# Kernel tuning notes

Measured on AMD Instinct MI355X. Metric: run time of the kernel, lower is better.

The kernel has to match this reference:

```python
import jax, jax.numpy as jnp
import numpy as np

B, S, IN_C, OUT_C = 2, 1024, 4096, 32000


def setup_inputs() -> dict:
    key = jax.random.key(0)
    k1, k2, k3 = jax.random.split(key, 3)
    hidden_states = jax.random.normal(k1, (B, S, IN_C), dtype=jnp.float32)
    weight = jax.random.normal(k2, (OUT_C, IN_C), dtype=jnp.float32) * 0.02
    bias = jax.random.normal(k3, (OUT_C,), dtype=jnp.float32) * 0.02
    return {"hidden_states": hidden_states, "weight": weight, "bias": bias,
            "split_num": 2}


def reference(hidden_states, weight, bias, split_num):
    # SlicedLMHead: split in_features into `split_num` contiguous slices,
    # run each slice as a linear to outC, accumulate, then add bias.
    in_c = hidden_states.shape[-1]
    split_size = in_c // split_num // 2 * 2
    logits = None
    for i in range(split_num):
        start = i * split_size
        end = (i + 1) * split_size if i < split_num - 1 else in_c
        h_slice = hidden_states[:, :, start:end]          # [B, S, slice]
        w_slice = weight[:, start:end]                    # [outC, slice]
        logits_slice = jnp.einsum('bsc,vc->bsv', h_slice, w_slice)
        logits = logits_slice if logits is None else logits + logits_slice
    return logits + bias
```

## Files before the change

kernel.cpp:

```cpp
#include <hip/hip_runtime.h>
#include <hip/hip_bf16.h>


typedef __attribute__((ext_vector_type(8))) short bhalf8;
typedef __attribute__((ext_vector_type(4))) float f32x4;
typedef __attribute__((ext_vector_type(8))) unsigned short us8;

#define M_DIM 2048
#define N_DIM 32000
#define K_DIM 4096
#define BM 256
#define BN 256
#define BK 64
#define NT (K_DIM / BK)
#define MBLKS (M_DIM / BM)
#define NBLKS (N_DIM / BN)
#define NWG (MBLKS * NBLKS)

#define W_ELEMS ((size_t)N_DIM * K_DIM)
#define H_ELEMS ((size_t)M_DIM * K_DIM)
#define WS_NEEDED ((W_ELEMS + H_ELEMS) * 2)

#define GLOAD_LDS16(g, l) \
    __builtin_amdgcn_global_load_lds( \
        (const __attribute__((address_space(1))) unsigned int*)(g), \
        (__attribute__((address_space(3))) unsigned int*)(l), 16, 0, 0)

__device__ __forceinline__ unsigned short f2bf_rn(float f) {
    unsigned int u = __float_as_uint(f);
    u += 0x7FFFu + ((u >> 16) & 1u);
    return (unsigned short)(u >> 16);
}

__global__ __launch_bounds__(256)
void cvt_f32_bf16(const float* __restrict__ in, unsigned short* __restrict__ out,
                  size_t n8) {
    size_t i = (size_t)blockIdx.x * blockDim.x + threadIdx.x;
    const size_t stride = (size_t)gridDim.x * blockDim.x;
    for (; i < n8; i += stride) {
        const float4 v0 = ((const float4*)in)[i * 2];
        const float4 v1 = ((const float4*)in)[i * 2 + 1];
        us8 p;
        p[0] = f2bf_rn(v0.x); p[1] = f2bf_rn(v0.y);
        p[2] = f2bf_rn(v0.z); p[3] = f2bf_rn(v0.w);
        p[4] = f2bf_rn(v1.x); p[5] = f2bf_rn(v1.y);
        p[6] = f2bf_rn(v1.z); p[7] = f2bf_rn(v1.w);
        ((us8*)out)[i] = p;
    }
}

__global__ __launch_bounds__(512, 2)
void lmhead_gemm_256(const unsigned short* __restrict__ A,
                     const unsigned short* __restrict__ W,
                     const float* __restrict__ bias,
                     float* __restrict__ C)
{
    __shared__ unsigned short lds[65536];

    const int tid  = threadIdx.x;
    const int bid  = blockIdx.x;
    const int wgid = (bid & 7) * (NWG / 8) + (bid >> 3);
    const int mblk = wgid & (MBLKS - 1);
    const int nblk = wgid >> 3;

    const int lane = tid & 63;
    const int wv   = tid >> 6;
    const int wr   = wv >> 2;
    const int wc   = wv & 3;
    const int l15  = lane & 15;
    const int l4   = lane >> 4;

    const int strow = tid >> 3;
    const int sgsw  = ((tid & 7) ^ (strow & 7)) << 3;
    const unsigned short* const srcA = A + (size_t)(mblk * BM + strow) * K_DIM + sgsw;
    const unsigned short* const srcB = W + (size_t)(nblk * BN + strow) * K_DIM + sgsw;
    const int dstw = (tid & 448) * 8;

#define STAGE_A(u, h) { \
        const unsigned short* s_ = srcA + (size_t)((h) * 128) * K_DIM + (size_t)(u) * BK; \
        unsigned short* d_ = &lds[((((u) & 1) * 2 + (h)) * 8192) + dstw]; \
        GLOAD_LDS16(s_, d_); GLOAD_LDS16(s_ + (size_t)64 * K_DIM, d_ + 4096); }
#define STAGE_B(u, h) { \
        const unsigned short* s_ = srcB + (size_t)((h) * 128) * K_DIM + (size_t)(u) * BK; \
        unsigned short* d_ = &lds[32768 + ((((u) & 1) * 2 + (h)) * 8192) + dstw]; \
        GLOAD_LDS16(s_, d_); GLOAD_LDS16(s_ + (size_t)64 * K_DIM, d_ + 4096); }

    const int swz0  = (l4 ^ (l15 & 7)) << 3;
    const int swz1  = ((4 + l4) ^ (l15 & 7)) << 3;
    const int aoff0 = l15 * 64 + swz0;
    const int aoff1 = l15 * 64 + swz1;
    const int boff0 = ((wc & 1) * 64 + l15) * 64 + swz0;
    const int boff1 = ((wc & 1) * 64 + l15) * 64 + swz1;

    f32x4 acc[8][4] = {};
    bhalf8 af0[4][2], af1[4][2], bf[4][2];

    STAGE_A(0, 0); STAGE_A(0, 1);
    STAGE_B(0, 0); STAGE_B(0, 1);
    STAGE_A(1, 0); STAGE_A(1, 1);
    asm volatile("s_waitcnt vmcnt(4)" ::: "memory");
    __builtin_amdgcn_sched_barrier(0);
    __builtin_amdgcn_s_barrier();

    for (int t = 0; t < NT; ++t) {
        const int b = t & 1;
        const unsigned short* asb = &lds[(b * 2 + wr) * 8192];
        const unsigned short* bsb = &lds[32768 + (b * 2 + (wc >> 1)) * 8192];

        #pragma unroll
        for (int mf = 0; mf < 4; ++mf) {
            af0[mf][0] = *(const bhalf8*)&asb[aoff0 + mf * 1024];
            af0[mf][1] = *(const bhalf8*)&asb[aoff1 + mf * 1024];
        }
        #pragma unroll
        for (int nf = 0; nf < 2; ++nf) {
            bf[nf][0] = *(const bhalf8*)&bsb[boff0 + nf * 1024];
            bf[nf][1] = *(const bhalf8*)&bsb[boff1 + nf * 1024];
        }
        if (t + 1 < NT) STAGE_B(t + 1, 0);
        __builtin_amdgcn_sched_barrier(0);
        __builtin_amdgcn_s_barrier();
        asm volatile("s_waitcnt lgkmcnt(0)" ::: "memory");
        __builtin_amdgcn_sched_barrier(0);
        __builtin_amdgcn_s_setprio(1);
        #pragma unroll
        for (int mf = 0; mf < 4; ++mf)
            #pragma unroll
            for (int nf = 0; nf < 2; ++nf)
                #pragma unroll
                for (int kk = 0; kk < 2; ++kk)
                    acc[mf][nf] = __builtin_amdgcn_mfma_f32_16x16x32_bf16(
                        af0[mf][kk], bf[nf][kk], acc[mf][nf], 0, 0, 0);
        __builtin_amdgcn_s_setprio(0);
        __builtin_amdgcn_s_barrier();

        #pragma unroll
        for (int nf = 0; nf < 2; ++nf) {
            bf[2 + nf][0] = *(const bhalf8*)&bsb[boff0 + (2 + nf) * 1024];
            bf[2 + nf][1] = *(const bhalf8*)&bsb[boff1 + (2 + nf) * 1024];
        }
        if (t + 1 < NT) STAGE_B(t + 1, 1);
        __builtin_amdgcn_sched_barrier(0);
        __builtin_amdgcn_s_barrier();
        asm volatile("s_waitcnt lgkmcnt(0)" ::: "memory");
        __builtin_amdgcn_sched_barrier(0);
        __builtin_amdgcn_s_setprio(1);
        #pragma unroll
        for (int mf = 0; mf < 4; ++mf)
            #pragma unroll
            for (int nf = 0; nf < 2; ++nf)
                #pragma unroll
                for (int kk = 0; kk < 2; ++kk)
                    acc[mf][2 + nf] = __builtin_amdgcn_mfma_f32_16x16x32_bf16(
                        af0[mf][kk], bf[2 + nf][kk], acc[mf][2 + nf], 0, 0, 0);
        __builtin_amdgcn_s_setprio(0);
        __builtin_amdgcn_s_barrier();

        #pragma unroll
        for (int mf = 0; mf < 4; ++mf) {
            af1[mf][0] = *(const bhalf8*)&asb[aoff0 + 4096 + mf * 1024];
            af1[mf][1] = *(const bhalf8*)&asb[aoff1 + 4096 + mf * 1024];
        }
        __builtin_amdgcn_sched_barrier(0);
        __builtin_amdgcn_s_barrier();
        asm volatile("s_waitcnt lgkmcnt(0)" ::: "memory");
        __builtin_amdgcn_sched_barrier(0);
        __builtin_amdgcn_s_setprio(1);
        #pragma unroll
        for (int mf = 0; mf < 4; ++mf)
            #pragma unroll
            for (int nf = 0; nf < 2; ++nf)
                #pragma unroll
                for (int kk = 0; kk < 2; ++kk)
                    acc[4 + mf][2 + nf] = __builtin_amdgcn_mfma_f32_16x16x32_bf16(
                        af1[mf][kk], bf[2 + nf][kk], acc[4 + mf][2 + nf], 0, 0, 0);
        __builtin_amdgcn_s_setprio(0);
        __builtin_amdgcn_s_barrier();

        if (t + 2 < NT) { STAGE_A(t + 2, 0); STAGE_A(t + 2, 1); }
        __builtin_amdgcn_sched_barrier(0);
        __builtin_amdgcn_s_barrier();
        __builtin_amdgcn_s_setprio(1);
        #pragma unroll
        for (int mf = 0; mf < 4; ++mf)
            #pragma unroll
            for (int nf = 0; nf < 2; ++nf)
                #pragma unroll
                for (int kk = 0; kk < 2; ++kk)
                    acc[4 + mf][nf] = __builtin_amdgcn_mfma_f32_16x16x32_bf16(
                        af1[mf][kk], bf[nf][kk], acc[4 + mf][nf], 0, 0, 0);
        __builtin_amdgcn_s_setprio(0);
        if (t < NT - 2) { asm volatile("s_waitcnt vmcnt(4)" ::: "memory"); }
        else            { asm volatile("s_waitcnt vmcnt(0)" ::: "memory"); }
        __builtin_amdgcn_sched_barrier(0);
        __builtin_amdgcn_s_barrier();
    }

    const size_t crow0 = (size_t)(mblk * BM + wr * 128 + l4 * 4);
    const int    ccol0 = nblk * BN + wc * 64 + l15;
    #pragma unroll
    for (int jn = 0; jn < 4; ++jn) {
        const float bv = bias[ccol0 + jn * 16];
        #pragma unroll
        for (int i = 0; i < 8; ++i) {
            const size_t base = (crow0 + (size_t)i * 16) * N_DIM + ccol0 + jn * 16;
            #pragma unroll
            for (int r = 0; r < 4; ++r)
                C[base + (size_t)r * N_DIM] = acc[i][jn][r] + bv;
        }
    }
#undef STAGE_A
#undef STAGE_B
}

__global__ __launch_bounds__(256, 2)
void lmhead_gemm_f32(const float* __restrict__ A, const float* __restrict__ W,
                     const float* __restrict__ bias, float* __restrict__ C) {
    __shared__ unsigned short As[2][128 * 64];
    __shared__ unsigned short Bs[2][128 * 64];

    const int tid  = threadIdx.x;
    const int bid  = blockIdx.x;
    const int mblk = bid & 15;
    const int nblk = bid >> 4;
    const int st_row = tid >> 3;
    const int st_g   = tid & 7;
    const int lane = tid & 63;
    const int wv   = tid >> 6;
    const int wm   = (wv >> 1) << 6;
    const int wn   = (wv & 1) << 6;
    const int l15  = lane & 15;
    const int l4   = lane >> 4;

    const float* aptr = A + (size_t)(mblk * 128 + st_row) * K_DIM + st_g * 8;
    const float* bptr = W + (size_t)(nblk * 128 + st_row) * K_DIM + st_g * 8;

    f32x4 acc[4][4] = {};
    float4 ra[4][2], rb[4][2];

    #pragma unroll
    for (int s = 0; s < 4; ++s) {
        const float* ap = aptr + (size_t)(s * 32) * K_DIM;
        const float* bp = bptr + (size_t)(s * 32) * K_DIM;
        ra[s][0] = *(const float4*)(ap);   ra[s][1] = *(const float4*)(ap + 4);
        rb[s][0] = *(const float4*)(bp);   rb[s][1] = *(const float4*)(bp + 4);
    }
    #pragma unroll
    for (int s = 0; s < 4; ++s) {
        const int row = s * 32 + st_row;
        const int off = row * 64 + ((st_g ^ (row & 7)) << 3);
        us8 pa, pb;
        #pragma unroll
        for (int j = 0; j < 4; ++j) {
            pa[j] = f2bf_rn(((const float*)&ra[s][0])[j]);
            pa[j + 4] = f2bf_rn(((const float*)&ra[s][1])[j]);
            pb[j] = f2bf_rn(((const float*)&rb[s][0])[j]);
            pb[j + 4] = f2bf_rn(((const float*)&rb[s][1])[j]);
        }
        *(us8*)&As[0][off] = pa;  *(us8*)&Bs[0][off] = pb;
    }
    __syncthreads();

    for (int t = 0; t < 64; ++t) {
        const int cur = t & 1;
        const bool more = (t + 1) < 64;
        if (more) {
            const float* ap = aptr + (size_t)(t + 1) * 64;
            const float* bp = bptr + (size_t)(t + 1) * 64;
            #pragma unroll
            for (int s = 0; s < 4; ++s) {
                ra[s][0] = *(const float4*)(ap + (size_t)(s * 32) * K_DIM);
                ra[s][1] = *(const float4*)(ap + (size_t)(s * 32) * K_DIM + 4);
                rb[s][0] = *(const float4*)(bp + (size_t)(s * 32) * K_DIM);
                rb[s][1] = *(const float4*)(bp + (size_t)(s * 32) * K_DIM + 4);
            }
        }
        const unsigned short* as = As[cur];
        const unsigned short* bs = Bs[cur];
        #pragma unroll
        for (int kk = 0; kk < 2; ++kk) {
            bhalf8 af[4], bfv[4];
            #pragma unroll
            for (int mf = 0; mf < 4; ++mf) {
                const int row = wm + mf * 16 + l15;
                af[mf] = *(const bhalf8*)&as[row * 64 + ((((kk << 2) + l4) ^ (row & 7)) << 3)];
            }
            #pragma unroll
            for (int nf = 0; nf < 4; ++nf) {
                const int row = wn + nf * 16 + l15;
                bfv[nf] = *(const bhalf8*)&bs[row * 64 + ((((kk << 2) + l4) ^ (row & 7)) << 3)];
            }
            #pragma unroll
            for (int mf = 0; mf < 4; ++mf)
                #pragma unroll
                for (int nf = 0; nf < 4; ++nf)
                    acc[mf][nf] = __builtin_amdgcn_mfma_f32_16x16x32_bf16(
                        af[mf], bfv[nf], acc[mf][nf], 0, 0, 0);
        }
        if (more) {
            const int nbuf = cur ^ 1;
            #pragma unroll
            for (int s = 0; s < 4; ++s) {
                const int row = s * 32 + st_row;
                const int off = row * 64 + ((st_g ^ (row & 7)) << 3);
                us8 pa, pb;
                #pragma unroll
                for (int j = 0; j < 4; ++j) {
                    pa[j] = f2bf_rn(((const float*)&ra[s][0])[j]);
                    pa[j + 4] = f2bf_rn(((const float*)&ra[s][1])[j]);
                    pb[j] = f2bf_rn(((const float*)&rb[s][0])[j]);
                    pb[j + 4] = f2bf_rn(((const float*)&rb[s][1])[j]);
                }
                *(us8*)&As[nbuf][off] = pa;  *(us8*)&Bs[nbuf][off] = pb;
            }
        }
        __syncthreads();
    }

    const size_t crow0 = (size_t)(mblk * 128 + wm + l4 * 4);
    const int    ccol0 = nblk * 128 + wn + l15;
    #pragma unroll
    for (int nf = 0; nf < 4; ++nf) {
        const float bv = bias[ccol0 + nf * 16];
        #pragma unroll
        for (int mf = 0; mf < 4; ++mf) {
            const size_t base = (crow0 + (size_t)mf * 16) * N_DIM + ccol0 + nf * 16;
            #pragma unroll
            for (int r = 0; r < 4; ++r)
                C[base + (size_t)r * N_DIM] = acc[mf][nf][r] + bv;
        }
    }
}

extern "C" void kernel_launch(void* const* d_in, const int* in_sizes, int n_in,
                              void* d_out, int out_size, void* d_ws, size_t ws_size,
                              hipStream_t stream) {
    const float* h = (const float*)d_in[0];
    const float* w = (const float*)d_in[1];
    const float* b = (const float*)d_in[2];
    float* out = (float*)d_out;

    if (ws_size >= WS_NEEDED) {
        unsigned short* wbf = (unsigned short*)d_ws;
        unsigned short* hbf = wbf + W_ELEMS;
        cvt_f32_bf16<<<2048, 256, 0, stream>>>(w, wbf, W_ELEMS / 8);
        cvt_f32_bf16<<<512, 256, 0, stream>>>(h, hbf, H_ELEMS / 8);
        lmhead_gemm_256<<<NWG, 512, 0, stream>>>(hbf, wbf, b, out);
    } else {
        lmhead_gemm_f32<<<4000, 256, 0, stream>>>(h, w, b, out);
    }
}
```

Measured before the change: 629.5 us.

## Restructure bf16 GEMM main loop into register double-buffered k-half pipeline

Replaces the four-phase per-tile schedule, which had many barriers and staggered A/B staging, with a two-half scheme. Fragments for the next k-half are read from LDS into a second register set while 32 MFMAs run on the current set. Whole tiles are staged two ahead, with one barrier per tile. The output is written with nontemporal stores to avoid polluting cache. This adds fragment registers, which risks spills or lower occupancy, and it waits vmcnt(0) every tile, which may expose global load latency.

Measured after the change: 1.998 ms. +217.4%, slower.

```diff
diff --git a/kernel.cpp b/kernel.cpp
--- a/kernel.cpp
+++ b/kernel.cpp
@@ -76,141 +76,101 @@
     const unsigned short* const srcB = W + (size_t)(nblk * BN + strow) * K_DIM + sgsw;
     const int dstw = (tid & 448) * 8;
 
-#define STAGE_A(u, h) { \
+#define STAGE_A(u, h, BUF) { \
         const unsigned short* s_ = srcA + (size_t)((h) * 128) * K_DIM + (size_t)(u) * BK; \
-        unsigned short* d_ = &lds[((((u) & 1) * 2 + (h)) * 8192) + dstw]; \
+        unsigned short* d_ = &lds[(((BUF) * 2 + (h)) * 8192) + dstw]; \
         GLOAD_LDS16(s_, d_); GLOAD_LDS16(s_ + (size_t)64 * K_DIM, d_ + 4096); }
-#define STAGE_B(u, h) { \
+#define STAGE_B(u, h, BUF) { \
         const unsigned short* s_ = srcB + (size_t)((h) * 128) * K_DIM + (size_t)(u) * BK; \
-        unsigned short* d_ = &lds[32768 + ((((u) & 1) * 2 + (h)) * 8192) + dstw]; \
+        unsigned short* d_ = &lds[32768 + (((BUF) * 2 + (h)) * 8192) + dstw]; \
         GLOAD_LDS16(s_, d_); GLOAD_LDS16(s_ + (size_t)64 * K_DIM, d_ + 4096); }
-
-    const int swz0  = (l4 ^ (l15 & 7)) << 3;
-    const int swz1  = ((4 + l4) ^ (l15 & 7)) << 3;
-    const int aoff0 = l15 * 64 + swz0;
-    const int aoff1 = l15 * 64 + swz1;
-    const int boff0 = ((wc & 1) * 64 + l15) * 64 + swz0;
-    const int boff1 = ((wc & 1) * 64 + l15) * 64 + swz1;
+#define STAGE_TILE(u, BUF) { \
+        STAGE_A(u, 0, BUF); STAGE_A(u, 1, BUF); \
+        STAGE_B(u, 0, BUF); STAGE_B(u, 1, BUF); }
+
+    const int swz0 = (l4 ^ (l15 & 7)) << 3;
+    const int swz1 = ((4 + l4) ^ (l15 & 7)) << 3;
+    const int arow = l15 * 64;
+    const int brow = ((wc & 1) * 64 + l15) * 64;
+
+    const unsigned short* const asp[2] = { &lds[wr * 8192],
+                                           &lds[(2 + wr) * 8192] };
+    const unsigned short* const bsp[2] = { &lds[32768 + (wc >> 1) * 8192],
+                                           &lds[32768 + (2 + (wc >> 1)) * 8192] };
 
     f32x4 acc[8][4] = {};
-    bhalf8 af0[4][2], af1[4][2], bf[4][2];
-
-    STAGE_A(0, 0); STAGE_A(0, 1);
-    STAGE_B(0, 0); STAGE_B(0, 1);
-    STAGE_A(1, 0); STAGE_A(1, 1);
-    asm volatile("s_waitcnt vmcnt(4)" ::: "memory");
+    bhalf8 aA[8], bA[4];
+    bhalf8 aB[8], bB[4];
+
+#define ISSUE_FRAGS(av, bv, as_, bs_, swz) { \
+        const unsigned short* _as = (as_); const unsigned short* _bs = (bs_); \
+        _Pragma("unroll") \
+        for (int i = 0; i < 4; ++i) av[i]     = *(const bhalf8*)&_as[arow + (swz) + i * 1024]; \
+        _Pragma("unroll") \
+        for (int i = 0; i < 4; ++i) av[4 + i] = *(const bhalf8*)&_as[arow + (swz) + 4096 + i * 1024]; \
+        _Pragma("unroll") \
+        for (int j = 0; j < 4; ++j) bv[j]     = *(const bhalf8*)&_bs[brow + (swz) + j * 1024]; }
+
+#define MFMA32(av, bv) { \
+        _Pragma("unroll") \
+        for (int i = 0; i < 8; ++i) \
+            _Pragma("unroll") \
+            for (int j = 0; j < 4; ++j) \
+                acc[i][j] = __builtin_amdgcn_mfma_f32_16x16x32_bf16(av[i], bv[j], acc[i][j], 0, 0, 0); }
+
+    STAGE_TILE(0, 0);
+    STAGE_TILE(1, 1);
+    asm volatile("s_waitcnt vmcnt(8)" ::: "memory");
     __builtin_amdgcn_sched_barrier(0);
     __builtin_amdgcn_s_barrier();
-
-    for (int t = 0; t < NT; ++t) {
-        const int b = t & 1;
-        const unsigned short* asb = &lds[(b * 2 + wr) * 8192];
-        const unsigned short* bsb = &lds[32768 + (b * 2 + (wc >> 1)) * 8192];
-
-        #pragma unroll
-        for (int mf = 0; mf < 4; ++mf) {
-            af0[mf][0] = *(const bhalf8*)&asb[aoff0 + mf * 1024];
-            af0[mf][1] = *(const bhalf8*)&asb[aoff1 + mf * 1024];
-        }
-        #pragma unroll
-        for (int nf = 0; nf < 2; ++nf) {
-            bf[nf][0] = *(const bhalf8*)&bsb[boff0 + nf * 1024];
-            bf[nf][1] = *(const bhalf8*)&bsb[boff1 + nf * 1024];
-        }
-        if (t + 1 < NT) STAGE_B(t + 1, 0);
-        __builtin_amdgcn_sched_barrier(0);
-        __builtin_amdgcn_s_barrier();
-        asm volatile("s_waitcnt lgkmcnt(0)" ::: "memory");
-        __builtin_amdgcn_sched_barrier(0);
-        __builtin_amdgcn_s_setprio(1);
-        #pragma unroll
-        for (int mf = 0; mf < 4; ++mf)
-            #pragma unroll
-            for (int nf = 0; nf < 2; ++nf)
-                #pragma unroll
-                for (int kk = 0; kk < 2; ++kk)
-                    acc[mf][nf] = __builtin_amdgcn_mfma_f32_16x16x32_bf16(
-                        af0[mf][kk], bf[nf][kk], acc[mf][nf], 0, 0, 0);
-        __builtin_amdgcn_s_setprio(0);
-        __builtin_amdgcn_s_barrier();
-
-        #pragma unroll
-        for (int nf = 0; nf < 2; ++nf) {
-            bf[2 + nf][0] = *(const bhalf8*)&bsb[boff0 + (2 + nf) * 1024];
-            bf[2 + nf][1] = *(const bhalf8*)&bsb[boff1 + (2 + nf) * 1024];
-        }
-        if (t + 1 < NT) STAGE_B(t + 1, 1);
-        __builtin_amdgcn_sched_barrier(0);
-        __builtin_amdgcn_s_barrier();
-        asm volatile("s_waitcnt lgkmcnt(0)" ::: "memory");
-        __builtin_amdgcn_sched_barrier(0);
-        __builtin_amdgcn_s_setprio(1);
-        #pragma unroll
-        for (int mf = 0; mf < 4; ++mf)
-            #pragma unroll
-            for (int nf = 0; nf < 2; ++nf)
-                #pragma unroll
-                for (int kk = 0; kk < 2; ++kk)
-                    acc[mf][2 + nf] = __builtin_amdgcn_mfma_f32_16x16x32_bf16(
-                        af0[mf][kk], bf[2 + nf][kk], acc[mf][2 + nf], 0, 0, 0);
-        __builtin_amdgcn_s_setprio(0);
-        __builtin_amdgcn_s_barrier();
-
-        #pragma unroll
-        for (int mf = 0; mf < 4; ++mf) {
-            af1[mf][0] = *(const bhalf8*)&asb[aoff0 + 4096 + mf * 1024];
-            af1[mf][1] = *(const bhalf8*)&asb[aoff1 + 4096 + mf * 1024];
-        }
-        __builtin_amdgcn_sched_barrier(0);
-        __builtin_amdgcn_s_barrier();
-        asm volatile("s_waitcnt lgkmcnt(0)" ::: "memory");
-        __builtin_amdgcn_sched_barrier(0);
-        __builtin_amdgcn_s_setprio(1);
-        #pragma unroll
-        for (int mf = 0; mf < 4; ++mf)
-            #pragma unroll
-            for (int nf = 0; nf < 2; ++nf)
-                #pragma unroll
-                for (int kk = 0; kk < 2; ++kk)
-                    acc[4 + mf][2 + nf] = __builtin_amdgcn_mfma_f32_16x16x32_bf16(
-                        af1[mf][kk], bf[2 + nf][kk], acc[4 + mf][2 + nf], 0, 0, 0);
-        __builtin_amdgcn_s_setprio(0);
-        __builtin_amdgcn_s_barrier();
-
-        if (t + 2 < NT) { STAGE_A(t + 2, 0); STAGE_A(t + 2, 1); }
-        __builtin_amdgcn_sched_barrier(0);
-        __builtin_amdgcn_s_barrier();
-        __builtin_amdgcn_s_setprio(1);
-        #pragma unroll
-        for (int mf = 0; mf < 4; ++mf)
-            #pragma unroll
-            for (int nf = 0; nf < 2; ++nf)
-                #pragma unroll
-                for (int kk = 0; kk < 2; ++kk)
-                    acc[4 + mf][nf] = __builtin_amdgcn_mfma_f32_16x16x32_bf16(
-                        af1[mf][kk], bf[nf][kk], acc[4 + mf][nf], 0, 0, 0);
-        __builtin_amdgcn_s_setprio(0);
-        if (t < NT - 2) { asm volatile("s_waitcnt vmcnt(4)" ::: "memory"); }
-        else            { asm volatile("s_waitcnt vmcnt(0)" ::: "memory"); }
-        __builtin_amdgcn_sched_barrier(0);
-        __builtin_amdgcn_s_barrier();
+    ISSUE_FRAGS(aA, bA, asp[0], bsp[0], swz0);
+
+#define TILE_STEP(T, B) { \
+         \
+        ISSUE_FRAGS(aB, bB, asp[B], bsp[B], swz1); \
+        __builtin_amdgcn_sched_barrier(0); \
+        asm volatile("s_waitcnt lgkmcnt(12)" ::: "memory"); \
+        __builtin_amdgcn_sched_barrier(0); \
+        __builtin_amdgcn_s_setprio(1); \
+        MFMA32(aA, bA); \
+        __builtin_amdgcn_s_setprio(0); \
+         \
+        asm volatile("s_waitcnt vmcnt(0) lgkmcnt(0)" ::: "memory"); \
+        __builtin_amdgcn_sched_barrier(0); \
+        __builtin_amdgcn_s_barrier(); \
+        if ((T) + 2 < NT) STAGE_TILE((T) + 2, B); \
+        if ((T) + 1 < NT) ISSUE_FRAGS(aA, bA, asp[B ^ 1], bsp[B ^ 1], swz0); \
+        __builtin_amdgcn_sched_barrier(0); \
+        __builtin_amdgcn_s_setprio(1); \
+        MFMA32(aB, bB); \
+        __builtin_amdgcn_s_setprio(0); }
+
+    #pragma unroll 1
+    for (int t = 0; t < NT; t += 2) {
+        TILE_STEP(t, 0);
+        TILE_STEP(t + 1, 1);
     }
 
     const size_t crow0 = (size_t)(mblk * BM + wr * 128 + l4 * 4);
     const int    ccol0 = nblk * BN + wc * 64 + l15;
     #pragma unroll
-    for (int jn = 0; jn < 4; ++jn) {
-        const float bv = bias[ccol0 + jn * 16];
+    for (int j = 0; j < 4; ++j) {
+        const float bv = bias[ccol0 + j * 16];
         #pragma unroll
         for (int i = 0; i < 8; ++i) {
-            const size_t base = (crow0 + (size_t)i * 16) * N_DIM + ccol0 + jn * 16;
+            const size_t base = (crow0 + (size_t)i * 16) * N_DIM + ccol0 + j * 16;
             #pragma unroll
             for (int r = 0; r < 4; ++r)
-                C[base + (size_t)r * N_DIM] = acc[i][jn][r] + bv;
+                __builtin_nontemporal_store(acc[i][j][r] + bv,
+                                            &C[base + (size_t)r * N_DIM]);
         }
     }
 #undef STAGE_A
 #undef STAGE_B
+#undef STAGE_TILE
+#undef ISSUE_FRAGS
+#undef MFMA32
+#undef TILE_STEP
 }
 
 __global__ __launch_bounds__(256, 2)
```

## Prefetch next A fragments across iterations and relax LDS waits in GEMM loop

Applied to the files above, without the earlier changes.

Restructures the bf16 MFMA main loop so the first A fragments for the next K-tile are loaded from LDS at the end of the current iteration, and all B fragments are loaded up front. Full lgkmcnt(0) waits become partial waits (lgkmcnt(4), lgkmcnt(8)), and several s_barriers are removed, so MFMA quadrants can start while later LDS reads are still in flight. The MFMA quadrant order is changed to reuse the fragments already in registers, and loop unrolling is disabled. This adds register pressure and relies on the fewer barriers still keeping the LDS double buffering race-free.

Result: no change. 620.7 us (-1.4%).

```diff
diff --git a/kernel.cpp b/kernel.cpp
--- a/kernel.cpp
+++ b/kernel.cpp
@@ -76,122 +76,131 @@
     const unsigned short* const srcB = W + (size_t)(nblk * BN + strow) * K_DIM + sgsw;
     const int dstw = (tid & 448) * 8;
 
-#define STAGE_A(u, h) { \
+#define STAGE_A(u, h, BUF) { \
         const unsigned short* s_ = srcA + (size_t)((h) * 128) * K_DIM + (size_t)(u) * BK; \
-        unsigned short* d_ = &lds[((((u) & 1) * 2 + (h)) * 8192) + dstw]; \
+        unsigned short* d_ = &lds[(((BUF) * 2 + (h)) * 8192) + dstw]; \
         GLOAD_LDS16(s_, d_); GLOAD_LDS16(s_ + (size_t)64 * K_DIM, d_ + 4096); }
-#define STAGE_B(u, h) { \
+#define STAGE_B(u, h, BUF) { \
         const unsigned short* s_ = srcB + (size_t)((h) * 128) * K_DIM + (size_t)(u) * BK; \
-        unsigned short* d_ = &lds[32768 + ((((u) & 1) * 2 + (h)) * 8192) + dstw]; \
+        unsigned short* d_ = &lds[32768 + (((BUF) * 2 + (h)) * 8192) + dstw]; \
         GLOAD_LDS16(s_, d_); GLOAD_LDS16(s_ + (size_t)64 * K_DIM, d_ + 4096); }
 
-    const int swz0  = (l4 ^ (l15 & 7)) << 3;
-    const int swz1  = ((4 + l4) ^ (l15 & 7)) << 3;
+    const int swz0 = (l4 ^ (l15 & 7)) << 3;
+    const int swz1 = ((4 + l4) ^ (l15 & 7)) << 3;
     const int aoff0 = l15 * 64 + swz0;
     const int aoff1 = l15 * 64 + swz1;
     const int boff0 = ((wc & 1) * 64 + l15) * 64 + swz0;
     const int boff1 = ((wc & 1) * 64 + l15) * 64 + swz1;
 
     f32x4 acc[8][4] = {};
-    bhalf8 af0[4][2], af1[4][2], bf[4][2];
-
-    STAGE_A(0, 0); STAGE_A(0, 1);
-    STAGE_B(0, 0); STAGE_B(0, 1);
-    STAGE_A(1, 0); STAGE_A(1, 1);
+    bhalf8 af0[4][2], af1[4][2], bf01[2][2], bf23[2][2];
+
+    STAGE_A(0, 0, 0); STAGE_A(0, 1, 0);
+    STAGE_B(0, 0, 0); STAGE_B(0, 1, 0);
+    STAGE_A(1, 0, 1); STAGE_A(1, 1, 1);
     asm volatile("s_waitcnt vmcnt(4)" ::: "memory");
     __builtin_amdgcn_sched_barrier(0);
     __builtin_amdgcn_s_barrier();
-
+    {
+        const unsigned short* a0 = &lds[wr * 8192];
+        #pragma unroll
+        for (int i = 0; i < 4; ++i) {
+            af0[i][0] = *(const bhalf8*)&a0[aoff0 + i * 1024];
+            af0[i][1] = *(const bhalf8*)&a0[aoff1 + i * 1024];
+        }
+    }
+
+    #pragma unroll 1
     for (int t = 0; t < NT; ++t) {
         const int b = t & 1;
         const unsigned short* asb = &lds[(b * 2 + wr) * 8192];
         const unsigned short* bsb = &lds[32768 + (b * 2 + (wc >> 1)) * 8192];
-
-        #pragma unroll
-        for (int mf = 0; mf < 4; ++mf) {
-            af0[mf][0] = *(const bhalf8*)&asb[aoff0 + mf * 1024];
-            af0[mf][1] = *(const bhalf8*)&asb[aoff1 + mf * 1024];
-        }
-        #pragma unroll
-        for (int nf = 0; nf < 2; ++nf) {
-            bf[nf][0] = *(const bhalf8*)&bsb[boff0 + nf * 1024];
-            bf[nf][1] = *(const bhalf8*)&bsb[boff1 + nf * 1024];
-        }
-        if (t + 1 < NT) STAGE_B(t + 1, 0);
-        __builtin_amdgcn_sched_barrier(0);
-        __builtin_amdgcn_s_barrier();
-        asm volatile("s_waitcnt lgkmcnt(0)" ::: "memory");
+        const unsigned short* asn = &lds[((b ^ 1) * 2 + wr) * 8192];
+
+        #pragma unroll
+        for (int j = 0; j < 2; ++j) {
+            bf01[j][0] = *(const bhalf8*)&bsb[boff0 + j * 1024];
+            bf01[j][1] = *(const bhalf8*)&bsb[boff1 + j * 1024];
+        }
+        #pragma unroll
+        for (int j = 0; j < 2; ++j) {
+            bf23[j][0] = *(const bhalf8*)&bsb[boff0 + (2 + j) * 1024];
+            bf23[j][1] = *(const bhalf8*)&bsb[boff1 + (2 + j) * 1024];
+        }
+        if (t + 1 < NT) STAGE_B(t + 1, 0, b ^ 1);
+        __builtin_amdgcn_sched_barrier(0);
+        asm volatile("s_waitcnt lgkmcnt(4)" ::: "memory");
         __builtin_amdgcn_sched_barrier(0);
         __builtin_amdgcn_s_setprio(1);
         #pragma unroll
-        for (int mf = 0; mf < 4; ++mf)
-            #pragma unroll
-            for (int nf = 0; nf < 2; ++nf)
+        for (int i = 0; i < 4; ++i)
+            #pragma unroll
+            for (int j = 0; j < 2; ++j)
                 #pragma unroll
                 for (int kk = 0; kk < 2; ++kk)
-                    acc[mf][nf] = __builtin_amdgcn_mfma_f32_16x16x32_bf16(
-                        af0[mf][kk], bf[nf][kk], acc[mf][nf], 0, 0, 0);
+                    acc[i][j] = __builtin_amdgcn_mfma_f32_16x16x32_bf16(
+                        af0[i][kk], bf01[j][kk], acc[i][j], 0, 0, 0);
         __builtin_amdgcn_s_setprio(0);
         __builtin_amdgcn_s_barrier();
 
         #pragma unroll
-        for (int nf = 0; nf < 2; ++nf) {
-            bf[2 + nf][0] = *(const bhalf8*)&bsb[boff0 + (2 + nf) * 1024];
-            bf[2 + nf][1] = *(const bhalf8*)&bsb[boff1 + (2 + nf) * 1024];
-        }
-        if (t + 1 < NT) STAGE_B(t + 1, 1);
-        __builtin_amdgcn_sched_barrier(0);
-        __builtin_amdgcn_s_barrier();
-        asm volatile("s_waitcnt lgkmcnt(0)" ::: "memory");
+        for (int i = 0; i < 4; ++i) {
+            af1[i][0] = *(const bhalf8*)&asb[aoff0 + 4096 + i * 1024];
+            af1[i][1] = *(const bhalf8*)&asb[aoff1 + 4096 + i * 1024];
+        }
+        if (t + 1 < NT) STAGE_B(t + 1, 1, b ^ 1);
+        __builtin_amdgcn_sched_barrier(0);
+        asm volatile("s_waitcnt lgkmcnt(8)" ::: "memory");
         __builtin_amdgcn_sched_barrier(0);
         __builtin_amdgcn_s_setprio(1);
         #pragma unroll
-        for (int mf = 0; mf < 4; ++mf)
-            #pragma unroll
-            for (int nf = 0; nf < 2; ++nf)
+        for (int i = 0; i < 4; ++i)
+            #pragma unroll
+            for (int j = 0; j < 2; ++j)
                 #pragma unroll
                 for (int kk = 0; kk < 2; ++kk)
-                    acc[mf][2 + nf] = __builtin_amdgcn_mfma_f32_16x16x32_bf16(
-                        af0[mf][kk], bf[2 + nf][kk], acc[mf][2 + nf], 0, 0, 0);
+                    acc[i][2 + j] = __builtin_amdgcn_mfma_f32_16x16x32_bf16(
+                        af0[i][kk], bf23[j][kk], acc[i][2 + j], 0, 0, 0);
         __builtin_amdgcn_s_setprio(0);
         __builtin_amdgcn_s_barrier();
 
-        #pragma unroll
-        for (int mf = 0; mf < 4; ++mf) {
-            af1[mf][0] = *(const bhalf8*)&asb[aoff0 + 4096 + mf * 1024];
-            af1[mf][1] = *(const bhalf8*)&asb[aoff1 + 4096 + mf * 1024];
-        }
-        __builtin_amdgcn_sched_barrier(0);
-        __builtin_amdgcn_s_barrier();
         asm volatile("s_waitcnt lgkmcnt(0)" ::: "memory");
         __builtin_amdgcn_sched_barrier(0);
         __builtin_amdgcn_s_setprio(1);
         #pragma unroll
-        for (int mf = 0; mf < 4; ++mf)
-            #pragma unroll
-            for (int nf = 0; nf < 2; ++nf)
+        for (int i = 0; i < 4; ++i)
+            #pragma unroll
+            for (int j = 0; j < 2; ++j)
                 #pragma unroll
                 for (int kk = 0; kk < 2; ++kk)
-                    acc[4 + mf][2 + nf] = __builtin_amdgcn_mfma_f32_16x16x32_bf16(
-                        af1[mf][kk], bf[2 + nf][kk], acc[4 + mf][2 + nf], 0, 0, 0);
+                    acc[4 + i][j] = __builtin_amdgcn_mfma_f32_16x16x32_bf16(
+                        af1[i][kk], bf01[j][kk], acc[4 + i][j], 0, 0, 0);
         __builtin_amdgcn_s_setprio(0);
         __builtin_amdgcn_s_barrier();
 
-        if (t + 2 < NT) { STAGE_A(t + 2, 0); STAGE_A(t + 2, 1); }
-        __builtin_amdgcn_sched_barrier(0);
-        __builtin_amdgcn_s_barrier();
+        if (t + 2 < NT) { STAGE_A(t + 2, 0, b); STAGE_A(t + 2, 1, b); }
+        __builtin_amdgcn_sched_barrier(0);
         __builtin_amdgcn_s_setprio(1);
         #pragma unroll
-        for (int mf = 0; mf < 4; ++mf)
-            #pragma unroll
-            for (int nf = 0; nf < 2; ++nf)
+        for (int i = 0; i < 4; ++i)
+            #pragma unroll
+            for (int j = 0; j < 2; ++j)
                 #pragma unroll
                 for (int kk = 0; kk < 2; ++kk)
-                    acc[4 + mf][nf] = __builtin_amdgcn_mfma_f32_16x16x32_bf16(
-                        af1[mf][kk], bf[nf][kk], acc[4 + mf][nf], 0, 0, 0);
+                    acc[4 + i][2 + j] = __builtin_amdgcn_mfma_f32_16x16x32_bf16(
+                        af1[i][kk], bf23[j][kk], acc[4 + i][2 + j], 0, 0, 0);
         __builtin_amdgcn_s_setprio(0);
+        __builtin_amdgcn_sched_barrier(0);
         if (t < NT - 2) { asm volatile("s_waitcnt vmcnt(4)" ::: "memory"); }
         else            { asm volatile("s_waitcnt vmcnt(0)" ::: "memory"); }
+        __builtin_amdgcn_sched_barrier(0);
+        if (t + 1 < NT) {
+            #pragma unroll
+            for (int i = 0; i < 4; ++i) {
+                af0[i][0] = *(const bhalf8*)&asn[aoff0 + i * 1024];
+                af0[i][1] = *(const bhalf8*)&asn[aoff1 + i * 1024];
+            }
+        }
         __builtin_amdgcn_sched_barrier(0);
         __builtin_amdgcn_s_barrier();
     }
@@ -199,14 +208,14 @@
     const size_t crow0 = (size_t)(mblk * BM + wr * 128 + l4 * 4);
     const int    ccol0 = nblk * BN + wc * 64 + l15;
     #pragma unroll
-    for (int jn = 0; jn < 4; ++jn) {
-        const float bv = bias[ccol0 + jn * 16];
+    for (int j = 0; j < 4; ++j) {
+        const float bv = bias[ccol0 + j * 16];
         #pragma unroll
         for (int i = 0; i < 8; ++i) {
-            const size_t base = (crow0 + (size_t)i * 16) * N_DIM + ccol0 + jn * 16;
+            const size_t base = (crow0 + (size_t)i * 16) * N_DIM + ccol0 + j * 16;
             #pragma unroll
             for (int r = 0; r < 4; ++r)
-                C[base + (size_t)r * N_DIM] = acc[i][jn][r] + bv;
+                C[base + (size_t)r * N_DIM] = acc[i][j][r] + bv;
         }
     }
 #undef STAGE_A
```
